# Performance work log

Measured on AMD Instinct MI355X. Metric: run time of the kernel, lower is better.

Reference implementation:

```python
import jax, jax.numpy as jnp
import numpy as np

N_NODES = 50000


def gcn_conv(x, W, b, src, dst, ew, n):
    """PyG-style GCNConv: D^-1/2 (A+I) D^-1/2 X W + b with self-loops of weight 1."""
    h = x @ W                                   # [N, out]
    loop = jnp.arange(n, dtype=src.dtype)
    s = jnp.concatenate([src, loop])            # [E+N]
    d = jnp.concatenate([dst, loop])
    w = jnp.concatenate([ew, jnp.ones((n,), dtype=x.dtype)])
    deg = jax.ops.segment_sum(w, d, num_segments=n)
    dinv = jnp.where(deg > 0, jax.lax.rsqrt(deg), 0.0)
    norm = dinv[s] * w * dinv[d]                # [E+N]
    out = jax.ops.segment_sum(h[s] * norm[:, None], d, num_segments=n)
    return out + b


def setup_inputs() -> dict:
    key = jax.random.key(0)
    ks = jax.random.split(key, 12)
    in_feats, hidden = 128, 128
    half = hidden // 2
    E = 800000
    x = jax.random.normal(ks[0], (N_NODES, in_feats), dtype=jnp.float32)
    edge_index = jax.random.randint(ks[1], (2, E), 0, N_NODES, dtype=jnp.int64)
    edge_weight = jax.random.uniform(ks[2], (E,), dtype=jnp.float32)
    def lin(k, fan_in, shape):
        bound = 1.0 / np.sqrt(fan_in)
        return jax.random.uniform(k, shape, minval=-bound, maxval=bound, dtype=jnp.float32)
    return {
        "x": x,
        "edge_index": edge_index,
        "edge_weight": edge_weight,
        "W1": lin(ks[3], in_feats, (in_feats, hidden)),
        "b1": jnp.zeros((hidden,), jnp.float32),
        "W2": lin(ks[4], hidden, (hidden, hidden)),
        "b2": jnp.zeros((hidden,), jnp.float32),
        "Ws": lin(ks[5], in_feats, (in_feats, hidden)),
        "bs": lin(ks[6], in_feats, (hidden,)),
        "Wl": lin(ks[7], in_feats, (in_feats, half)),
        "bl": jnp.zeros((half,), jnp.float32),
        "Wl2": lin(ks[8], half, (half, 1)),
        "bl2": lin(ks[9], half, (1,)),
    }


def reference(x, edge_index, edge_weight, W1, b1, W2, b2, Ws, bs, Wl, bl, Wl2, bl2):
    n = x.shape[0]
    src, dst = edge_index[0], edge_index[1]
    # conv1 + ReLU over neighbors
    h_neighbors = jax.nn.relu(gcn_conv(x, W1, b1, src, dst, edge_weight, n))
    # leader score: GCNConv -> ReLU -> Linear(.,1) -> sigmoid, per node
    ls_h = jax.nn.relu(gcn_conv(x, Wl, bl, src, dst, edge_weight, n))
    leader_score = jax.nn.sigmoid(ls_h @ Wl2 + bl2)        # [N, 1]
    # gated fusion of self projection vs neighbor aggregation
    h_self_proj = x @ Ws + bs
    h_new = (1.0 - leader_score) * h_neighbors + leader_score * h_self_proj
    h_final = jax.nn.relu(gcn_conv(h_new, W2, b2, src, dst, edge_weight, n))
    return (h_final, leader_score)
```

## Files before the change

### kernel.cpp

```cpp
#include <hip/hip_runtime.h>
#include <math.h>

#define THREADS 256
#define ELLS 96

typedef unsigned int uint32;
typedef unsigned long long ull64;
typedef __attribute__((ext_vector_type(8))) short bf16x8;
typedef __attribute__((ext_vector_type(4))) float f32x4;
typedef __attribute__((ext_vector_type(2))) float f32x2;

__device__ __forceinline__ unsigned short f2bf_rne(float x) {
  uint32 u = __float_as_uint(x);
  u += 0x7fffu + ((u >> 16) & 1u);
  return (unsigned short)(u >> 16);
}

__device__ __forceinline__ f32x2 dw2f2(uint32 d) {
  f32x2 r;
  r.x = __uint_as_float(d << 16);
  r.y = __uint_as_float(d & 0xffff0000u);
  return r;
}


__global__ __launch_bounds__(256) void prep_fused(ull64* __restrict__ packed, int n,
                                                  const float* __restrict__ W1, const float* __restrict__ Wl,
                                                  const float* __restrict__ Ws, const float* __restrict__ W2,
                                                  unsigned short* __restrict__ whi, unsigned short* __restrict__ wlo,
                                                  int nInit) {
  int b = blockIdx.x;
  int t = threadIdx.x;
  if (b < nInit) {
    int i = b * 256 + t;
    if (i < n) packed[i] = 0ull;
  } else {
    int idx = (b - nInit) * 256 + t;
    if (idx >= 448 * 128) return;
    int slot = idx >> 7;
    int k = idx & 127;
    const float* W; int ncol, ncols;
    if (slot < 128)      { W = W1; ncol = slot;       ncols = 128; }
    else if (slot < 192) { W = Wl; ncol = slot - 128; ncols = 64;  }
    else if (slot < 320) { W = Ws; ncol = slot - 192; ncols = 128; }
    else                 { W = W2; ncol = slot - 320; ncols = 128; }
    float v = W[(size_t)k * ncols + ncol];
    unsigned short hi = f2bf_rne(v);
    float hif = __uint_as_float((uint32)hi << 16);
    unsigned short lo = f2bf_rne(v - hif);
    whi[idx] = hi;
    wlo[idx] = lo;
  }
}


__global__ __launch_bounds__(THREADS) void edge_scatter_kernel(const int* __restrict__ ei, const float* __restrict__ ew,
                                                               ull64* __restrict__ packed,
                                                               int2* __restrict__ ell, int E) {
  int e = blockIdx.x * THREADS + threadIdx.x;
  if (e >= E) return;
  int s = ei[e];
  int d = ei[E + e];
  float w = ew[e];
  uint32 fx = (uint32)(w * 8388608.0f + 0.5f);
  ull64 old = atomicAdd(packed + d, (1ull << 32) | (ull64)fx);
  int slot = (int)(old >> 32);
  if (slot < ELLS)
    ell[(size_t)d * ELLS + slot] = make_int2(s, __float_as_int(w));
}


__global__ __launch_bounds__(256) void cast_kernel(const ull64* __restrict__ packed,
                                                   const float* __restrict__ x,
                                                   float* __restrict__ dinv, int* __restrict__ cnt32,
                                                   unsigned short* __restrict__ xraw,
                                                   unsigned short* __restrict__ xscl, int n8) {
  int i = blockIdx.x * 256 + threadIdx.x;
  if (i >= n8) return;
  int row = i >> 4;
  const float S = 1.1920928955078125e-7f;
  ull64 p = packed[row];
  float di = rsqrtf(1.0f + (float)(uint32)(p & 0xffffffffull) * S);
  if ((i & 15) == 0) {
    dinv[row] = di;
    cnt32[row] = (int)(p >> 32);
  }
  const float* px = x + (size_t)i * 8;
  float4 a = *(const float4*)px;
  float4 c = *(const float4*)(px + 4);
  ushort4 r0, r1, s0, s1;
  r0.x = f2bf_rne(a.x); r0.y = f2bf_rne(a.y); r0.z = f2bf_rne(a.z); r0.w = f2bf_rne(a.w);
  r1.x = f2bf_rne(c.x); r1.y = f2bf_rne(c.y); r1.z = f2bf_rne(c.z); r1.w = f2bf_rne(c.w);
  s0.x = f2bf_rne(di * a.x); s0.y = f2bf_rne(di * a.y); s0.z = f2bf_rne(di * a.z); s0.w = f2bf_rne(di * a.w);
  s1.x = f2bf_rne(di * c.x); s1.y = f2bf_rne(di * c.y); s1.z = f2bf_rne(di * c.z); s1.w = f2bf_rne(di * c.w);
  *(ushort4*)(xraw + (size_t)i * 8) = r0;
  *(ushort4*)(xraw + (size_t)i * 8 + 4) = r1;
  *(ushort4*)(xscl + (size_t)i * 8) = s0;
  *(ushort4*)(xscl + (size_t)i * 8 + 4) = s1;
}


struct Chunk {
  const unsigned short* A;
  const unsigned short* whi;
  const unsigned short* wlo;
  const float* bias;
  void* out;
  int ostride;
  int obf16;
};
struct GemmArgs { Chunk c[5]; };

__global__ __launch_bounds__(256, 2) void gemm_v3(GemmArgs args, int M, int nTiles) {
  Chunk d = args.c[blockIdx.x];
  const unsigned short* A = d.A;
  int w = threadIdx.x >> 6, lane = threadIdx.x & 63;
  int n16 = lane & 15, quad = lane >> 4;

  bf16x8 Bh[4][4], Bl[4][4];
  {
    const unsigned short* wh = d.whi + (size_t)n16 * 128 + quad * 8;
    const unsigned short* wl = d.wlo + (size_t)n16 * 128 + quad * 8;
#pragma unroll
    for (int ct = 0; ct < 4; ct++)
#pragma unroll
      for (int ks = 0; ks < 4; ks++) {
        Bh[ct][ks] = *(const bf16x8*)(wh + ct * 16 * 128 + ks * 32);
        Bl[ct][ks] = *(const bf16x8*)(wl + ct * 16 * 128 + ks * 32);
      }
  }
  float bv[4];
#pragma unroll
  for (int ct = 0; ct < 4; ct++) bv[ct] = d.bias ? d.bias[ct * 16 + n16] : 0.f;

  int tile = blockIdx.y;
  bf16x8 av0[4], av1[4];
  if (tile < nTiles) {
    int bm = tile * 128;
    int r0 = bm + w * 32 + n16, r1 = r0 + 16;
    int r0c = r0 < M ? r0 : M - 1;
    int r1c = r1 < M ? r1 : M - 1;
    const unsigned short* a0 = A + (size_t)r0c * 128 + quad * 8;
    const unsigned short* a1 = A + (size_t)r1c * 128 + quad * 8;
#pragma unroll
    for (int ks = 0; ks < 4; ks++) {
      av0[ks] = *(const bf16x8*)(a0 + ks * 32);
      av1[ks] = *(const bf16x8*)(a1 + ks * 32);
    }
  }

  for (; tile < nTiles; tile += gridDim.y) {
    int nxt = tile + gridDim.y;
    bf16x8 nv0[4], nv1[4];
    if (nxt < nTiles) {
      int bm = nxt * 128;
      int r0 = bm + w * 32 + n16, r1 = r0 + 16;
      int r0c = r0 < M ? r0 : M - 1;
      int r1c = r1 < M ? r1 : M - 1;
      const unsigned short* a0 = A + (size_t)r0c * 128 + quad * 8;
      const unsigned short* a1 = A + (size_t)r1c * 128 + quad * 8;
#pragma unroll
      for (int ks = 0; ks < 4; ks++) {
        nv0[ks] = *(const bf16x8*)(a0 + ks * 32);
        nv1[ks] = *(const bf16x8*)(a1 + ks * 32);
      }
    }

    f32x4 acc[2][4];
#pragma unroll
    for (int rt = 0; rt < 2; rt++)
#pragma unroll
      for (int ct = 0; ct < 4; ct++) acc[rt][ct] = (f32x4){0.f, 0.f, 0.f, 0.f};

#pragma unroll
    for (int ks = 0; ks < 4; ks++)
#pragma unroll
      for (int ct = 0; ct < 4; ct++) {
        acc[0][ct] = __builtin_amdgcn_mfma_f32_16x16x32_bf16(av0[ks], Bh[ct][ks], acc[0][ct], 0, 0, 0);
        acc[0][ct] = __builtin_amdgcn_mfma_f32_16x16x32_bf16(av0[ks], Bl[ct][ks], acc[0][ct], 0, 0, 0);
        acc[1][ct] = __builtin_amdgcn_mfma_f32_16x16x32_bf16(av1[ks], Bh[ct][ks], acc[1][ct], 0, 0, 0);
        acc[1][ct] = __builtin_amdgcn_mfma_f32_16x16x32_bf16(av1[ks], Bl[ct][ks], acc[1][ct], 0, 0, 0);
      }

    int bm = tile * 128;
#pragma unroll
    for (int ct = 0; ct < 4; ct++) {
      int col = ct * 16 + n16;
#pragma unroll
      for (int rt = 0; rt < 2; rt++) {
#pragma unroll
        for (int reg = 0; reg < 4; reg++) {
          int row = bm + w * 32 + rt * 16 + quad * 4 + reg;
          if (row < M) {
            float v = acc[rt][ct][reg] + bv[ct];
            if (d.obf16)
              ((unsigned short*)d.out)[(size_t)row * d.ostride + col] = f2bf_rne(v);
            else
              ((float*)d.out)[(size_t)row * d.ostride + col] = v;
          }
        }
      }
    }

#pragma unroll
    for (int ks = 0; ks < 4; ks++) { av0[ks] = nv0[ks]; av1[ks] = nv1[ks]; }
  }
}


__global__ __launch_bounds__(256) void conv1_fused(const unsigned short* __restrict__ h1,
                                                   const unsigned short* __restrict__ hl,
                                                   const int* __restrict__ cnt,
                                                   const int2* __restrict__ csr,
                                                   const float* __restrict__ dinv,
                                                   const float* __restrict__ b1, const float* __restrict__ bl,
                                                   const float* __restrict__ Wl2, const float* __restrict__ bl2,
                                                   const unsigned short* __restrict__ hself,
                                                   unsigned short* __restrict__ hnew_out,
                                                   float* __restrict__ leader_out, int nnodes) {
  int wave = threadIdx.x >> 6;
  int lane = threadIdx.x & 63;
  int node = blockIdx.x * 4 + wave;
  if (node >= nnodes) return;
  int g = lane >> 4, q = lane & 15;
  bool ql = q < 8;
  int rs = node * ELLS;
  int n = cnt[node];
  float di = dinv[node];

  f32x2 acc1[4] = {};
  f32x2 accl[4] = {};
  if (g == 0) {
    uint4 v = *(const uint4*)(h1 + (size_t)node * 128 + 8 * q);
    acc1[0] = dw2f2(v.x); acc1[1] = dw2f2(v.y);
    acc1[2] = dw2f2(v.z); acc1[3] = dw2f2(v.w);
    if (ql) {
      uint4 vl = *(const uint4*)(hl + (size_t)node * 64 + 8 * q);
      accl[0] = dw2f2(vl.x); accl[1] = dw2f2(vl.y);
      accl[2] = dw2f2(vl.z); accl[3] = dw2f2(vl.w);
    }
  }

  int e = g;
  for (; e + 4 < n; e += 8) {
    int2 en0 = csr[rs + e];
    int2 en1 = csr[rs + e + 4];
    f32x2 w0 = {__int_as_float(en0.y), __int_as_float(en0.y)};
    f32x2 w1 = {__int_as_float(en1.y), __int_as_float(en1.y)};
    uint4 a0 = *(const uint4*)(h1 + (size_t)en0.x * 128 + 8 * q);
    uint4 a1 = *(const uint4*)(h1 + (size_t)en1.x * 128 + 8 * q);
    if (ql) {
      uint4 c0 = *(const uint4*)(hl + (size_t)en0.x * 64 + 8 * q);
      uint4 c1 = *(const uint4*)(hl + (size_t)en1.x * 64 + 8 * q);
      accl[0] += w0 * dw2f2(c0.x) + w1 * dw2f2(c1.x);
      accl[1] += w0 * dw2f2(c0.y) + w1 * dw2f2(c1.y);
      accl[2] += w0 * dw2f2(c0.z) + w1 * dw2f2(c1.z);
      accl[3] += w0 * dw2f2(c0.w) + w1 * dw2f2(c1.w);
    }
    acc1[0] += w0 * dw2f2(a0.x) + w1 * dw2f2(a1.x);
    acc1[1] += w0 * dw2f2(a0.y) + w1 * dw2f2(a1.y);
    acc1[2] += w0 * dw2f2(a0.z) + w1 * dw2f2(a1.z);
    acc1[3] += w0 * dw2f2(a0.w) + w1 * dw2f2(a1.w);
  }
  if (e < n) {
    int2 en = csr[rs + e];
    f32x2 w0 = {__int_as_float(en.y), __int_as_float(en.y)};
    uint4 a0 = *(const uint4*)(h1 + (size_t)en.x * 128 + 8 * q);
    if (ql) {
      uint4 c0 = *(const uint4*)(hl + (size_t)en.x * 64 + 8 * q);
      accl[0] += w0 * dw2f2(c0.x);
      accl[1] += w0 * dw2f2(c0.y);
      accl[2] += w0 * dw2f2(c0.z);
      accl[3] += w0 * dw2f2(c0.w);
    }
    acc1[0] += w0 * dw2f2(a0.x);
    acc1[1] += w0 * dw2f2(a0.y);
    acc1[2] += w0 * dw2f2(a0.z);
    acc1[3] += w0 * dw2f2(a0.w);
  }

#pragma unroll
  for (int k = 0; k < 4; k++) {
    acc1[k].x += __shfl_xor(acc1[k].x, 16);
    acc1[k].y += __shfl_xor(acc1[k].y, 16);
    acc1[k].x += __shfl_xor(acc1[k].x, 32);
    acc1[k].y += __shfl_xor(acc1[k].y, 32);
    accl[k].x += __shfl_xor(accl[k].x, 16);
    accl[k].y += __shfl_xor(accl[k].y, 16);
    accl[k].x += __shfl_xor(accl[k].x, 32);
    accl[k].y += __shfl_xor(accl[k].y, 32);
  }

  float part = 0.f;
  if (ql) {
    float b[8], w2[8];
    *(float4*)&b[0] = *(const float4*)(bl + 8 * q);
    *(float4*)&b[4] = *(const float4*)(bl + 8 * q + 4);
    *(float4*)&w2[0] = *(const float4*)(Wl2 + 8 * q);
    *(float4*)&w2[4] = *(const float4*)(Wl2 + 8 * q + 4);
#pragma unroll
    for (int k = 0; k < 4; k++) {
      part += fmaxf(di * accl[k].x + b[2 * k], 0.f) * w2[2 * k];
      part += fmaxf(di * accl[k].y + b[2 * k + 1], 0.f) * w2[2 * k + 1];
    }
  }
  part += __shfl_xor(part, 1);
  part += __shfl_xor(part, 2);
  part += __shfl_xor(part, 4);
  float z = __shfl(part, 0) + bl2[0];
  float l = 1.f / (1.f + expf(-z));
  if (lane == 0) leader_out[node] = l;

  if (g == 0) {
    float b[8], r[8], hs[8];
    *(float4*)&b[0] = *(const float4*)(b1 + 8 * q);
    *(float4*)&b[4] = *(const float4*)(b1 + 8 * q + 4);
    uint4 hsv = *(const uint4*)(hself + (size_t)node * 128 + 8 * q);
    f32x2 h0 = dw2f2(hsv.x), h1v = dw2f2(hsv.y), h2v = dw2f2(hsv.z), h3v = dw2f2(hsv.w);
    hs[0] = h0.x; hs[1] = h0.y; hs[2] = h1v.x; hs[3] = h1v.y;
    hs[4] = h2v.x; hs[5] = h2v.y; hs[6] = h3v.x; hs[7] = h3v.y;
    float a[8];
    a[0] = acc1[0].x; a[1] = acc1[0].y; a[2] = acc1[1].x; a[3] = acc1[1].y;
    a[4] = acc1[2].x; a[5] = acc1[2].y; a[6] = acc1[3].x; a[7] = acc1[3].y;
#pragma unroll
    for (int j = 0; j < 8; j++) {
      r[j] = fmaxf(di * a[j] + b[j], 0.f);
      r[j] = (1.f - l) * r[j] + l * hs[j];
      r[j] *= di;
    }
    ushort4 p0, p1;
    p0.x = f2bf_rne(r[0]); p0.y = f2bf_rne(r[1]); p0.z = f2bf_rne(r[2]); p0.w = f2bf_rne(r[3]);
    p1.x = f2bf_rne(r[4]); p1.y = f2bf_rne(r[5]); p1.z = f2bf_rne(r[6]); p1.w = f2bf_rne(r[7]);
    *(ushort4*)(hnew_out + (size_t)node * 128 + 8 * q) = p0;
    *(ushort4*)(hnew_out + (size_t)node * 128 + 8 * q + 4) = p1;
  }
}


__global__ __launch_bounds__(256) void agg_conv2_kernel(const unsigned short* __restrict__ h,
                                                        const int* __restrict__ cnt,
                                                        const int2* __restrict__ csr,
                                                        const float* __restrict__ dinv, const float* __restrict__ bias,
                                                        float* __restrict__ out, int nnodes) {
  int wave = threadIdx.x >> 6;
  int lane = threadIdx.x & 63;
  int node = blockIdx.x * 4 + wave;
  if (node >= nnodes) return;
  int g = lane >> 4;
  int q = lane & 15;
  int rs = node * ELLS;
  int n = cnt[node];
  float di = dinv[node];

  f32x2 acc[4] = {};
  if (g == 0) {
    uint4 v = *(const uint4*)(h + (size_t)node * 128 + 8 * q);
    acc[0] = dw2f2(v.x); acc[1] = dw2f2(v.y);
    acc[2] = dw2f2(v.z); acc[3] = dw2f2(v.w);
  }
  int e = g;
  for (; e + 4 < n; e += 8) {
    int2 en0 = csr[rs + e];
    int2 en1 = csr[rs + e + 4];
    f32x2 w0 = {__int_as_float(en0.y), __int_as_float(en0.y)};
    f32x2 w1 = {__int_as_float(en1.y), __int_as_float(en1.y)};
    uint4 v0 = *(const uint4*)(h + (size_t)en0.x * 128 + 8 * q);
    uint4 v1 = *(const uint4*)(h + (size_t)en1.x * 128 + 8 * q);
    acc[0] += w0 * dw2f2(v0.x) + w1 * dw2f2(v1.x);
    acc[1] += w0 * dw2f2(v0.y) + w1 * dw2f2(v1.y);
    acc[2] += w0 * dw2f2(v0.z) + w1 * dw2f2(v1.z);
    acc[3] += w0 * dw2f2(v0.w) + w1 * dw2f2(v1.w);
  }
  if (e < n) {
    int2 en = csr[rs + e];
    f32x2 w0 = {__int_as_float(en.y), __int_as_float(en.y)};
    uint4 v = *(const uint4*)(h + (size_t)en.x * 128 + 8 * q);
    acc[0] += w0 * dw2f2(v.x);
    acc[1] += w0 * dw2f2(v.y);
    acc[2] += w0 * dw2f2(v.z);
    acc[3] += w0 * dw2f2(v.w);
  }
#pragma unroll
  for (int k = 0; k < 4; k++) {
    acc[k].x += __shfl_xor(acc[k].x, 16);
    acc[k].y += __shfl_xor(acc[k].y, 16);
    acc[k].x += __shfl_xor(acc[k].x, 32);
    acc[k].y += __shfl_xor(acc[k].y, 32);
  }
  if (g == 0) {
    float b[8], r[8];
    *(float4*)&b[0] = *(const float4*)(bias + 8 * q);
    *(float4*)&b[4] = *(const float4*)(bias + 8 * q + 4);
    float a[8];
    a[0] = acc[0].x; a[1] = acc[0].y; a[2] = acc[1].x; a[3] = acc[1].y;
    a[4] = acc[2].x; a[5] = acc[2].y; a[6] = acc[3].x; a[7] = acc[3].y;
#pragma unroll
    for (int j = 0; j < 8; j++) r[j] = fmaxf(di * a[j] + b[j], 0.f);
    *(float4*)(out + (size_t)node * 128 + 8 * q) = *(float4*)&r[0];
    *(float4*)(out + (size_t)node * 128 + 8 * q + 4) = *(float4*)&r[4];
  }
}


extern "C" void kernel_launch(void* const* d_in, const int* in_sizes, int n_in,
                              void* d_out, int out_size, void* d_ws, size_t ws_size,
                              hipStream_t stream) {
  const float* x   = (const float*)d_in[0];
  const int*   ei  = (const int*)d_in[1];
  const float* ew  = (const float*)d_in[2];
  const float* W1  = (const float*)d_in[3];
  const float* b1  = (const float*)d_in[4];
  const float* W2  = (const float*)d_in[5];
  const float* b2  = (const float*)d_in[6];
  const float* Wsp = (const float*)d_in[7];
  const float* bs  = (const float*)d_in[8];
  const float* Wl  = (const float*)d_in[9];
  const float* bl  = (const float*)d_in[10];
  const float* Wl2 = (const float*)d_in[11];
  const float* bl2 = (const float*)d_in[12];

  const int N = in_sizes[0] / 128;
  const int E = in_sizes[1] / 2;

  char* ws = (char*)d_ws;
  size_t off = 0;
  auto alloc = [&](size_t bytes) -> void* {
    void* p = ws + off;
    off = (off + bytes + 255) & ~(size_t)255;
    return p;
  };
  ull64* packed    = (ull64*)alloc((size_t)N * 8);
  float* dinv      = (float*)alloc((size_t)N * 4);
  int*   cnt32     = (int*)alloc((size_t)N * 4);
  int2*  ell       = (int2*)alloc((size_t)N * ELLS * 8);
  unsigned short* xraw   = (unsigned short*)alloc((size_t)N * 128 * 2);
  unsigned short* xscl   = (unsigned short*)alloc((size_t)N * 128 * 2);
  unsigned short* h1bf   = (unsigned short*)alloc((size_t)N * 128 * 2);
  unsigned short* hlbf   = (unsigned short*)alloc((size_t)N * 64 * 2);
  unsigned short* hnewbf = (unsigned short*)alloc((size_t)N * 128 * 2);
  unsigned short* hspbf  = (unsigned short*)alloc((size_t)N * 128 * 2);
  unsigned short* whi = (unsigned short*)alloc((size_t)448 * 128 * 2);
  unsigned short* wlo = (unsigned short*)alloc((size_t)448 * 128 * 2);

  float* h_final = (float*)d_out;
  float* leader  = (float*)d_out + (size_t)N * 128;

  int gN = (N + THREADS - 1) / THREADS;
  int gE = (E + THREADS - 1) / THREADS;
  int gWave = (N + 3) / 4;
  int nTiles = (N + 127) / 128;
  int nCast = (N * 16 + 255) / 256;
  int nW = (448 * 128 + 255) / 256;

  prep_fused<<<gN + nW, 256, 0, stream>>>(packed, N, W1, Wl, Wsp, W2, whi, wlo, gN);
  edge_scatter_kernel<<<gE, THREADS, 0, stream>>>(ei, ew, packed, ell, E);
  cast_kernel<<<nCast, 256, 0, stream>>>(packed, x, dinv, cnt32, xraw, xscl, N * 16);

  {
    GemmArgs ga;
    ga.c[0] = {xscl, whi + 0 * 128,   wlo + 0 * 128,   nullptr, h1bf,       128, 1};
    ga.c[1] = {xscl, whi + 64 * 128,  wlo + 64 * 128,  nullptr, h1bf + 64,  128, 1};
    ga.c[2] = {xscl, whi + 128 * 128, wlo + 128 * 128, nullptr, hlbf,       64,  1};
    ga.c[3] = {xraw, whi + 192 * 128, wlo + 192 * 128, bs,      hspbf,      128, 1};
    ga.c[4] = {xraw, whi + 256 * 128, wlo + 256 * 128, bs + 64, hspbf + 64, 128, 1};
    gemm_v3<<<dim3(5, 104), 256, 0, stream>>>(ga, N, nTiles);
  }

  conv1_fused<<<gWave, 256, 0, stream>>>(h1bf, hlbf, cnt32, ell, dinv,
                                         b1, bl, Wl2, bl2, hspbf, hnewbf, leader, N);

  {
    GemmArgs ga;
    ga.c[0] = {hnewbf, whi + 320 * 128, wlo + 320 * 128, nullptr, h1bf,      128, 1};
    ga.c[1] = {hnewbf, whi + 384 * 128, wlo + 384 * 128, nullptr, h1bf + 64, 128, 1};
    ga.c[2] = ga.c[0]; ga.c[3] = ga.c[0]; ga.c[4] = ga.c[0];
    gemm_v3<<<dim3(2, 256), 256, 0, stream>>>(ga, N, nTiles);
  }
  agg_conv2_kernel<<<gWave, 256, 0, stream>>>(h1bf, cnt32, ell,
                                              dinv, b2, h_final, N);
}
```

Before: 284.5 us.

## Overlap edge scatter with first GEMM and move source-degree scaling into aggregation

Runs the first feature GEMM on unscaled bf16 x, so it no longer waits for node degrees. The edge scatter is folded into the same launch, with edge blocks interleaved between GEMM blocks so the atomic-heavy scatter overlaps the MFMA work. The source-side dinv scaling moves into the conv1 gather as an extra per-edge dinv lookup, which also removes the scaled x copy and the cast pass. The leader-score gather now uses all 16 lanes by splitting even and odd edges across half-groups, adding an extra shuffle reduction.

```diff
diff --git a/kernel.cpp b/kernel.cpp
--- a/kernel.cpp
+++ b/kernel.cpp
@@ -3,6 +3,8 @@
 
 #define THREADS 256
 #define ELLS 96
+#define NEDGEBLK 1024
+#define GEMM_YSTRIDE 104
 
 typedef unsigned int uint32;
 typedef unsigned long long ull64;
@@ -28,13 +30,14 @@
                                                   const float* __restrict__ W1, const float* __restrict__ Wl,
                                                   const float* __restrict__ Ws, const float* __restrict__ W2,
                                                   unsigned short* __restrict__ whi, unsigned short* __restrict__ wlo,
-                                                  int nInit) {
+                                                  const float* __restrict__ x, unsigned short* __restrict__ xraw,
+                                                  int nInit, int nW) {
   int b = blockIdx.x;
   int t = threadIdx.x;
   if (b < nInit) {
     int i = b * 256 + t;
     if (i < n) packed[i] = 0ull;
-  } else {
+  } else if (b < nInit + nW) {
     int idx = (b - nInit) * 256 + t;
     if (idx >= 448 * 128) return;
     int slot = idx >> 7;
@@ -50,53 +53,29 @@
     unsigned short lo = f2bf_rne(v - hif);
     whi[idx] = hi;
     wlo[idx] = lo;
-  }
-}
-
-
-__global__ __launch_bounds__(THREADS) void edge_scatter_kernel(const int* __restrict__ ei, const float* __restrict__ ew,
-                                                               ull64* __restrict__ packed,
-                                                               int2* __restrict__ ell, int E) {
-  int e = blockIdx.x * THREADS + threadIdx.x;
-  if (e >= E) return;
-  int s = ei[e];
-  int d = ei[E + e];
-  float w = ew[e];
-  uint32 fx = (uint32)(w * 8388608.0f + 0.5f);
-  ull64 old = atomicAdd(packed + d, (1ull << 32) | (ull64)fx);
-  int slot = (int)(old >> 32);
-  if (slot < ELLS)
-    ell[(size_t)d * ELLS + slot] = make_int2(s, __float_as_int(w));
-}
-
-
-__global__ __launch_bounds__(256) void cast_kernel(const ull64* __restrict__ packed,
-                                                   const float* __restrict__ x,
-                                                   float* __restrict__ dinv, int* __restrict__ cnt32,
-                                                   unsigned short* __restrict__ xraw,
-                                                   unsigned short* __restrict__ xscl, int n8) {
+  } else {
+    int i = (b - nInit - nW) * 256 + t;
+    if (i >= n * 16) return;
+    const float* px = x + (size_t)i * 8;
+    float4 a = *(const float4*)px;
+    float4 c = *(const float4*)(px + 4);
+    ushort4 r0, r1;
+    r0.x = f2bf_rne(a.x); r0.y = f2bf_rne(a.y); r0.z = f2bf_rne(a.z); r0.w = f2bf_rne(a.w);
+    r1.x = f2bf_rne(c.x); r1.y = f2bf_rne(c.y); r1.z = f2bf_rne(c.z); r1.w = f2bf_rne(c.w);
+    *(ushort4*)(xraw + (size_t)i * 8) = r0;
+    *(ushort4*)(xraw + (size_t)i * 8 + 4) = r1;
+  }
+}
+
+
+__global__ __launch_bounds__(256) void finalize_kernel(const ull64* __restrict__ packed,
+                                                       float* __restrict__ dinv, int* __restrict__ cnt32, int n) {
   int i = blockIdx.x * 256 + threadIdx.x;
-  if (i >= n8) return;
-  int row = i >> 4;
+  if (i >= n) return;
   const float S = 1.1920928955078125e-7f;
-  ull64 p = packed[row];
-  float di = rsqrtf(1.0f + (float)(uint32)(p & 0xffffffffull) * S);
-  if ((i & 15) == 0) {
-    dinv[row] = di;
-    cnt32[row] = (int)(p >> 32);
-  }
-  const float* px = x + (size_t)i * 8;
-  float4 a = *(const float4*)px;
-  float4 c = *(const float4*)(px + 4);
-  ushort4 r0, r1, s0, s1;
-  r0.x = f2bf_rne(a.x); r0.y = f2bf_rne(a.y); r0.z = f2bf_rne(a.z); r0.w = f2bf_rne(a.w);
-  r1.x = f2bf_rne(c.x); r1.y = f2bf_rne(c.y); r1.z = f2bf_rne(c.z); r1.w = f2bf_rne(c.w);
-  s0.x = f2bf_rne(di * a.x); s0.y = f2bf_rne(di * a.y); s0.z = f2bf_rne(di * a.z); s0.w = f2bf_rne(di * a.w);
-  s1.x = f2bf_rne(di * c.x); s1.y = f2bf_rne(di * c.y); s1.z = f2bf_rne(di * c.z); s1.w = f2bf_rne(di * c.w);
-  *(ushort4*)(xraw + (size_t)i * 8) = r0;
-  *(ushort4*)(xraw + (size_t)i * 8 + 4) = r1;
-  *(ushort4*)(xscl + (size_t)i * 8) = s0;
-  *(ushort4*)(xscl + (size_t)i * 8 + 4) = s1;
+  ull64 p = packed[i];
+  dinv[i] = rsqrtf(1.0f + (float)(uint32)(p & 0xffffffffull) * S);
+  cnt32[i] = (int)(p >> 32);
 }
 
 
@@ -111,8 +90,7 @@
 };
 struct GemmArgs { Chunk c[5]; };
 
-__global__ __launch_bounds__(256, 2) void gemm_v3(GemmArgs args, int M, int nTiles) {
-  Chunk d = args.c[blockIdx.x];
+__device__ __forceinline__ void gemm_body(const Chunk& d, int M, int nTiles, int tile0, int tstride) {
   const unsigned short* A = d.A;
   int w = threadIdx.x >> 6, lane = threadIdx.x & 63;
   int n16 = lane & 15, quad = lane >> 4;
@@ -133,7 +111,7 @@
 #pragma unroll
   for (int ct = 0; ct < 4; ct++) bv[ct] = d.bias ? d.bias[ct * 16 + n16] : 0.f;
 
-  int tile = blockIdx.y;
+  int tile = tile0;
   bf16x8 av0[4], av1[4];
   if (tile < nTiles) {
     int bm = tile * 128;
@@ -149,8 +127,8 @@
     }
   }
 
-  for (; tile < nTiles; tile += gridDim.y) {
-    int nxt = tile + gridDim.y;
+  for (; tile < nTiles; tile += tstride) {
+    int nxt = tile + tstride;
     bf16x8 nv0[4], nv1[4];
     if (nxt < nTiles) {
       int bm = nxt * 128;
@@ -205,6 +183,46 @@
 #pragma unroll
     for (int ks = 0; ks < 4; ks++) { av0[ks] = nv0[ks]; av1[ks] = nv1[ks]; }
   }
+}
+
+__global__ __launch_bounds__(256, 2) void gemm_v3(GemmArgs args, int M, int nTiles) {
+  gemm_body(args.c[blockIdx.x], M, nTiles, blockIdx.y, gridDim.y);
+}
+
+
+__global__ __launch_bounds__(256, 2) void fused_sg(GemmArgs args, int M, int nTiles, int nGemm,
+                                                   const int* __restrict__ ei, const float* __restrict__ ew,
+                                                   ull64* __restrict__ packed, int2* __restrict__ ell, int E) {
+  int b = blockIdx.x;
+  int gemmIdx = -1, edgeIdx = -1;
+  int twice = nGemm * 2;
+  if (b < twice) {
+    if (b & 1) gemmIdx = b >> 1; else edgeIdx = b >> 1;
+  } else {
+    edgeIdx = nGemm + (b - twice);
+  }
+
+  if (edgeIdx >= 0) {
+    int per = (E + NEDGEBLK - 1) / NEDGEBLK;
+    int start = edgeIdx * per;
+    int end = start + per;
+    if (end > E) end = E;
+    for (int e = start + (int)threadIdx.x; e < end; e += 256) {
+      int s = ei[e];
+      int d = ei[E + e];
+      float w = ew[e];
+      uint32 fx = (uint32)(w * 8388608.0f + 0.5f);
+      ull64 old = atomicAdd(packed + d, (1ull << 32) | (ull64)fx);
+      int slot = (int)(old >> 32);
+      if (slot < ELLS)
+        ell[(size_t)d * ELLS + slot] = make_int2(s, __float_as_int(w));
+    }
+    return;
+  }
+
+  int chunkId = gemmIdx % 5;
+  int ytile = gemmIdx / 5;
+  gemm_body(args.c[chunkId], M, nTiles, ytile, GEMM_YSTRIDE);
 }
 
 
@@ -224,20 +242,22 @@
   if (node >= nnodes) return;
   int g = lane >> 4, q = lane & 15;
   bool ql = q < 8;
+  int hq = q & 7;
   int rs = node * ELLS;
   int n = cnt[node];
   float di = dinv[node];
+  f32x2 dv2 = {di, di};
 
   f32x2 acc1[4] = {};
   f32x2 accl[4] = {};
   if (g == 0) {
     uint4 v = *(const uint4*)(h1 + (size_t)node * 128 + 8 * q);
-    acc1[0] = dw2f2(v.x); acc1[1] = dw2f2(v.y);
-    acc1[2] = dw2f2(v.z); acc1[3] = dw2f2(v.w);
+    acc1[0] = dv2 * dw2f2(v.x); acc1[1] = dv2 * dw2f2(v.y);
+    acc1[2] = dv2 * dw2f2(v.z); acc1[3] = dv2 * dw2f2(v.w);
     if (ql) {
       uint4 vl = *(const uint4*)(hl + (size_t)node * 64 + 8 * q);
-      accl[0] = dw2f2(vl.x); accl[1] = dw2f2(vl.y);
-      accl[2] = dw2f2(vl.z); accl[3] = dw2f2(vl.w);
+      accl[0] = dv2 * dw2f2(vl.x); accl[1] = dv2 * dw2f2(vl.y);
+      accl[2] = dv2 * dw2f2(vl.z); accl[3] = dv2 * dw2f2(vl.w);
     }
   }
 
@@ -245,18 +265,20 @@
   for (; e + 4 < n; e += 8) {
     int2 en0 = csr[rs + e];
     int2 en1 = csr[rs + e + 4];
-    f32x2 w0 = {__int_as_float(en0.y), __int_as_float(en0.y)};
-    f32x2 w1 = {__int_as_float(en1.y), __int_as_float(en1.y)};
+    float wz0 = __int_as_float(en0.y) * dinv[en0.x];
+    float wz1 = __int_as_float(en1.y) * dinv[en1.x];
+    f32x2 w0 = {wz0, wz0};
+    f32x2 w1 = {wz1, wz1};
     uint4 a0 = *(const uint4*)(h1 + (size_t)en0.x * 128 + 8 * q);
     uint4 a1 = *(const uint4*)(h1 + (size_t)en1.x * 128 + 8 * q);
-    if (ql) {
-      uint4 c0 = *(const uint4*)(hl + (size_t)en0.x * 64 + 8 * q);
-      uint4 c1 = *(const uint4*)(hl + (size_t)en1.x * 64 + 8 * q);
-      accl[0] += w0 * dw2f2(c0.x) + w1 * dw2f2(c1.x);
-      accl[1] += w0 * dw2f2(c0.y) + w1 * dw2f2(c1.y);
-      accl[2] += w0 * dw2f2(c0.z) + w1 * dw2f2(c1.z);
-      accl[3] += w0 * dw2f2(c0.w) + w1 * dw2f2(c1.w);
-    }
+    int srcl = ql ? en0.x : en1.x;
+    float wzl = ql ? wz0 : wz1;
+    uint4 c0 = *(const uint4*)(hl + (size_t)srcl * 64 + 8 * hq);
+    f32x2 wl2 = {wzl, wzl};
+    accl[0] += wl2 * dw2f2(c0.x);
+    accl[1] += wl2 * dw2f2(c0.y);
+    accl[2] += wl2 * dw2f2(c0.z);
+    accl[3] += wl2 * dw2f2(c0.w);
     acc1[0] += w0 * dw2f2(a0.x) + w1 * dw2f2(a1.x);
     acc1[1] += w0 * dw2f2(a0.y) + w1 * dw2f2(a1.y);
     acc1[2] += w0 * dw2f2(a0.z) + w1 * dw2f2(a1.z);
@@ -264,15 +286,16 @@
   }
   if (e < n) {
     int2 en = csr[rs + e];
-    f32x2 w0 = {__int_as_float(en.y), __int_as_float(en.y)};
+    float wz0 = __int_as_float(en.y) * dinv[en.x];
+    f32x2 w0 = {wz0, wz0};
     uint4 a0 = *(const uint4*)(h1 + (size_t)en.x * 128 + 8 * q);
-    if (ql) {
-      uint4 c0 = *(const uint4*)(hl + (size_t)en.x * 64 + 8 * q);
-      accl[0] += w0 * dw2f2(c0.x);
-      accl[1] += w0 * dw2f2(c0.y);
-      accl[2] += w0 * dw2f2(c0.z);
-      accl[3] += w0 * dw2f2(c0.w);
-    }
+    float wzl = ql ? wz0 : 0.f;
+    uint4 c0 = *(const uint4*)(hl + (size_t)en.x * 64 + 8 * hq);
+    f32x2 wl2 = {wzl, wzl};
+    accl[0] += wl2 * dw2f2(c0.x);
+    accl[1] += wl2 * dw2f2(c0.y);
+    accl[2] += wl2 * dw2f2(c0.z);
+    accl[3] += wl2 * dw2f2(c0.w);
     acc1[0] += w0 * dw2f2(a0.x);
     acc1[1] += w0 * dw2f2(a0.y);
     acc1[2] += w0 * dw2f2(a0.z);
@@ -289,6 +312,8 @@
     accl[k].y += __shfl_xor(accl[k].y, 16);
     accl[k].x += __shfl_xor(accl[k].x, 32);
     accl[k].y += __shfl_xor(accl[k].y, 32);
+    accl[k].x += __shfl_xor(accl[k].x, 8);
+    accl[k].y += __shfl_xor(accl[k].y, 8);
   }
 
   float part = 0.f;
@@ -434,7 +459,6 @@
   int*   cnt32     = (int*)alloc((size_t)N * 4);
   int2*  ell       = (int2*)alloc((size_t)N * ELLS * 8);
   unsigned short* xraw   = (unsigned short*)alloc((size_t)N * 128 * 2);
-  unsigned short* xscl   = (unsigned short*)alloc((size_t)N * 128 * 2);
   unsigned short* h1bf   = (unsigned short*)alloc((size_t)N * 128 * 2);
   unsigned short* hlbf   = (unsigned short*)alloc((size_t)N * 64 * 2);
   unsigned short* hnewbf = (unsigned short*)alloc((size_t)N * 128 * 2);
@@ -446,25 +470,26 @@
   float* leader  = (float*)d_out + (size_t)N * 128;
 
   int gN = (N + THREADS - 1) / THREADS;
-  int gE = (E + THREADS - 1) / THREADS;
   int gWave = (N + 3) / 4;
   int nTiles = (N + 127) / 128;
   int nCast = (N * 16 + 255) / 256;
   int nW = (448 * 128 + 255) / 256;
 
-  prep_fused<<<gN + nW, 256, 0, stream>>>(packed, N, W1, Wl, Wsp, W2, whi, wlo, gN);
-  edge_scatter_kernel<<<gE, THREADS, 0, stream>>>(ei, ew, packed, ell, E);
-  cast_kernel<<<nCast, 256, 0, stream>>>(packed, x, dinv, cnt32, xraw, xscl, N * 16);
+  prep_fused<<<gN + nW + nCast, 256, 0, stream>>>(packed, N, W1, Wl, Wsp, W2, whi, wlo, x, xraw, gN, nW);
 
   {
     GemmArgs ga;
-    ga.c[0] = {xscl, whi + 0 * 128,   wlo + 0 * 128,   nullptr, h1bf,       128, 1};
-    ga.c[1] = {xscl, whi + 64 * 128,  wlo + 64 * 128,  nullptr, h1bf + 64,  128, 1};
-    ga.c[2] = {xscl, whi + 128 * 128, wlo + 128 * 128, nullptr, hlbf,       64,  1};
+    ga.c[0] = {xraw, whi + 0 * 128,   wlo + 0 * 128,   nullptr, h1bf,       128, 1};
+    ga.c[1] = {xraw, whi + 64 * 128,  wlo + 64 * 128,  nullptr, h1bf + 64,  128, 1};
+    ga.c[2] = {xraw, whi + 128 * 128, wlo + 128 * 128, nullptr, hlbf,       64,  1};
     ga.c[3] = {xraw, whi + 192 * 128, wlo + 192 * 128, bs,      hspbf,      128, 1};
     ga.c[4] = {xraw, whi + 256 * 128, wlo + 256 * 128, bs + 64, hspbf + 64, 128, 1};
-    gemm_v3<<<dim3(5, 104), 256, 0, stream>>>(ga, N, nTiles);
-  }
+    int nGemm = 5 * GEMM_YSTRIDE;
+    int totalBlocks = nGemm * 2 + (NEDGEBLK - nGemm);
+    fused_sg<<<totalBlocks, 256, 0, stream>>>(ga, N, nTiles, nGemm, ei, ew, packed, ell, E);
+  }
+
+  finalize_kernel<<<gN, 256, 0, stream>>>(packed, dinv, cnt32, N);
 
   conv1_fused<<<gWave, 256, 0, stream>>>(h1bf, hlbf, cnt32, ell, dinv,
                                          b1, bl, Wl2, bl2, hspbf, hnewbf, leader, N);
```

After: 261.3 us. 1.09x faster.
